# Performance work log

Measured on AMD Instinct MI355X. Metric: run time of the kernel, lower is better.

The kernel has to match this reference:

```python
import jax, jax.numpy as jnp
import numpy as np
import math

NUM_HEADS = 16
ROPE_BASE = 10000.0


def _rope_tables(T, head_dim, dtype=jnp.float32):
    pos = jnp.arange(T, dtype=jnp.float32)
    inv_freq = 1.0 / (ROPE_BASE ** (jnp.arange(0, head_dim, 2, dtype=jnp.float32) / head_dim))
    ang = pos[:, None] * inv_freq[None, :]  # (T, D/2)
    return jnp.cos(ang).astype(dtype), jnp.sin(ang).astype(dtype)


def _apply_rope(x, cos, sin):
    # x: (B, T, H, D); rotate interleaved pairs, position indexed along T
    B, T, H, D = x.shape
    xr = x.reshape(B, T, H, D // 2, 2)
    xe, xo = xr[..., 0], xr[..., 1]
    c = cos[None, :, None, :]  # (1, T, 1, D/2)
    s = sin[None, :, None, :]
    re = xe * c - xo * s
    im = xe * s + xo * c
    return jnp.stack([re, im], axis=-1).reshape(B, T, H, D)


def setup_inputs() -> dict:
    key = jax.random.key(0)
    k1, k2, k3 = jax.random.split(key, 3)
    B, T, C = 2, 2048, 1024
    x = jax.random.normal(k1, (B, T, C), dtype=jnp.float32)
    w_qkv = jax.random.normal(k2, (C, 3 * C), dtype=jnp.float32) * (1.0 / math.sqrt(C))
    w_out = jax.random.normal(k3, (C, C), dtype=jnp.float32) * (1.0 / math.sqrt(C))
    return {"x": x, "w_qkv": w_qkv, "w_out": w_out}


def reference(x, w_qkv, w_out):
    B, T, C = x.shape
    H = NUM_HEADS
    D = C // H
    qkv = jnp.einsum('btc,cf->btf', x, w_qkv)  # (B, T, 3C)
    q, k, v = jnp.split(qkv, 3, axis=-1)
    q = q.reshape(B, T, H, D)
    k = k.reshape(B, T, H, D)
    v = v.reshape(B, T, H, D)
    cos, sin = _rope_tables(T, D)
    q = _apply_rope(q, cos, sin)
    k = _apply_rope(k, cos, sin)
    # (B, H, T, T) scores with causal mask
    att = jnp.einsum('bqhd,bkhd->bhqk', q, k) * (1.0 / math.sqrt(D))
    causal = jnp.tril(jnp.ones((T, T), dtype=bool))
    att = jnp.where(causal[None, None], att, -jnp.inf)
    att = jax.nn.softmax(att, axis=-1)
    out = jnp.einsum('bhqk,bkhd->bqhd', att, v).reshape(B, T, C)
    return jnp.einsum('btc,cd->btd', out, w_out)
```

## Files before the change

kernel.cpp:

```cpp
#include <hip/hip_runtime.h>
#include <stdint.h>


#define B_ 2
#define T_ 2048
#define C_ 1024
#define H_ 16
#define D_ 64
#define F_ 3072
#define M_ 4096

typedef unsigned short u16;
typedef unsigned int u32;
typedef u16 u16x2 __attribute__((ext_vector_type(2)));
typedef u16 u16x4 __attribute__((ext_vector_type(4)));
typedef u16 u16x8 __attribute__((ext_vector_type(8)));
typedef __bf16 bf16x8 __attribute__((ext_vector_type(8)));
typedef float f32x4 __attribute__((ext_vector_type(4)));

__device__ __forceinline__ float b2f(u16 u) {
  union { unsigned int i; float f; } v; v.i = ((unsigned int)u) << 16; return v.f;
}
__device__ __forceinline__ u16 f2b(float f) {
  unsigned int u = __float_as_uint(f);
  u += 0x7fffu + ((u >> 16) & 1u);
  return (u16)(u >> 16);
}
__device__ __forceinline__ bf16x8 u2b8(u16x8 v) {
  union { u16x8 u; bf16x8 b; } x; x.u = v; return x.b;
}


__global__ __launch_bounds__(256) void rope_table_kernel(float* cosT, float* sinT) {
  int idx = blockIdx.x * 256 + threadIdx.x;
  int t = idx >> 5, i = idx & 31;
  float inv_freq = powf(10000.0f, -(float)(2 * i) / 64.0f);
  float ang = (float)t * inv_freq;
  cosT[idx] = cosf(ang);
  sinT[idx] = sinf(ang);
}

__global__ __launch_bounds__(256) void cast_x_kernel(const float* __restrict__ x,
                                                     u16* __restrict__ xb) {
  int i = blockIdx.x * 256 + threadIdx.x;
  float4 v = ((const float4*)x)[i];
  u16x4 r;
  r[0] = f2b(v.x); r[1] = f2b(v.y); r[2] = f2b(v.z); r[3] = f2b(v.w);
  ((u16x4*)xb)[i] = r;
}

__global__ __launch_bounds__(256) void transpose_cast_kernel(const float* __restrict__ in,
                                                             u16* __restrict__ out,
                                                             int R, int Ccol) {
  __shared__ float tile[32][33];
  int c0 = blockIdx.x * 32, r0 = blockIdx.y * 32;
  int tx = threadIdx.x & 31, ty = threadIdx.x >> 5;
  #pragma unroll
  for (int i = 0; i < 32; i += 8)
    tile[ty + i][tx] = in[(size_t)(r0 + ty + i) * Ccol + c0 + tx];
  __syncthreads();
  #pragma unroll
  for (int i = 0; i < 32; i += 8)
    out[(size_t)(c0 + ty + i) * R + r0 + tx] = f2b(tile[tx][ty + i]);
}

template <typename TO>
__global__ __launch_bounds__(256) void gemm_bt_kernel(const u16* __restrict__ A,
                                                      const u16* __restrict__ Bt,
                                                      TO* __restrict__ Cm,
                                                      int M, int N, int K) {
  __shared__ u16 sA[2][128 * 32];
  __shared__ u16 sB[2][128 * 32];
  const int tid = threadIdx.x;
  const int lane = tid & 63;
  const int wv = tid >> 6;
  const int wr = wv >> 1, wc = wv & 1;
  const int l16 = lane & 15, lq = lane >> 4;
  const int rowBase = blockIdx.y * 128;
  const int colBase = blockIdx.x * 128;

  f32x4 acc[4][4] = {};

  const int e0 = wv * 1024 + lane * 8;

#define GSTAGE(buf, kk)                                                          \
  {                                                                              \
    _Pragma("unroll")                                                            \
    for (int s = 0; s < 2; ++s) {                                                \
      int e = e0 + s * 512;                                                      \
      int r = e >> 5, ccc = e & 31;                                              \
      __builtin_amdgcn_global_load_lds(                                          \
          (const __attribute__((address_space(1))) u32*)(A + (size_t)(rowBase + r) * K + (kk) + ccc), \
          (__attribute__((address_space(3))) u32*)&sA[buf][wv * 1024 + s * 512], 16, 0, 0); \
      __builtin_amdgcn_global_load_lds(                                          \
          (const __attribute__((address_space(1))) u32*)(Bt + (size_t)(colBase + r) * K + (kk) + ccc), \
          (__attribute__((address_space(3))) u32*)&sB[buf][wv * 1024 + s * 512], 16, 0, 0); \
    }                                                                            \
  }

  GSTAGE(0, 0);
  asm volatile("s_waitcnt vmcnt(0)" ::: "memory");
  __builtin_amdgcn_s_barrier();

  int cb = 0;
  for (int k0 = 0; k0 < K; k0 += 32, cb ^= 1) {
    const bool more = (k0 + 32 < K);
    if (more) {
      GSTAGE(cb ^ 1, k0 + 32);
      asm volatile("s_waitcnt vmcnt(4)" ::: "memory");
    } else {
      asm volatile("s_waitcnt vmcnt(0)" ::: "memory");
    }
    __builtin_amdgcn_s_barrier();

    bf16x8 af[4], bf[4];
    #pragma unroll
    for (int m = 0; m < 4; ++m)
      af[m] = u2b8(*(const u16x8*)&sA[cb][(wr * 64 + m * 16 + l16) * 32 + lq * 8]);
    #pragma unroll
    for (int n = 0; n < 4; ++n)
      bf[n] = u2b8(*(const u16x8*)&sB[cb][(wc * 64 + n * 16 + l16) * 32 + lq * 8]);
    __builtin_amdgcn_s_setprio(1);
    #pragma unroll
    for (int m = 0; m < 4; ++m)
      #pragma unroll
      for (int n = 0; n < 4; ++n)
        acc[m][n] = __builtin_amdgcn_mfma_f32_16x16x32_bf16(af[m], bf[n], acc[m][n], 0, 0, 0);
    __builtin_amdgcn_s_setprio(0);
    __builtin_amdgcn_s_barrier();
  }
#undef GSTAGE

  #pragma unroll
  for (int m = 0; m < 4; ++m) {
    #pragma unroll
    for (int n = 0; n < 4; ++n) {
      int row = rowBase + wr * 64 + m * 16 + lq * 4;
      int col = colBase + wc * 64 + n * 16 + l16;
      #pragma unroll
      for (int j = 0; j < 4; ++j) {
        float v = acc[m][n][j];
        if constexpr (sizeof(TO) == 2) {
          Cm[(size_t)(row + j) * N + col] = f2b(v);
        } else {
          Cm[(size_t)(row + j) * N + col] = v;
        }
      }
    }
  }
}

__global__ __launch_bounds__(256) void rope_reorg_kernel(const u16* __restrict__ qkv,
                                                         const float* __restrict__ cosT,
                                                         const float* __restrict__ sinT,
                                                         u16* __restrict__ qr,
                                                         u16* __restrict__ kr,
                                                         u16* __restrict__ vr) {
  const float QSC = 0.125f * 1.44269504f;
  int idx = blockIdx.x * 256 + threadIdx.x;
  int d2 = idx & 31;
  int h = (idx >> 5) & 15;
  int t = (idx >> 9) & 2047;
  int b = idx >> 20;
  size_t base = (size_t)(b * T_ + t) * F_ + h * 64 + d2 * 2;
  float qe = b2f(qkv[base]),        qo = b2f(qkv[base + 1]);
  float ke = b2f(qkv[base + C_]),   ko = b2f(qkv[base + C_ + 1]);
  float cv = cosT[t * 32 + d2], sv = sinT[t * 32 + d2];
  size_t ob = ((size_t)(b * H_ + h) * T_ + t) * D_ + d2 * 2;
  qr[ob]     = f2b((qe * cv - qo * sv) * QSC);
  qr[ob + 1] = f2b((qe * sv + qo * cv) * QSC);
  kr[ob]     = f2b(ke * cv - ko * sv);
  kr[ob + 1] = f2b(ke * sv + ko * cv);
  vr[ob]     = qkv[base + 2 * C_];
  vr[ob + 1] = qkv[base + 2 * C_ + 1];
}

__global__ __launch_bounds__(256, 4) void attn_mfma_kernel(const u16* __restrict__ qr,
                                                           const u16* __restrict__ kr,
                                                           const u16* __restrict__ vr,
                                                           u16* __restrict__ ao) {
  constexpr int LDK = 72, LDVT = 72;
  __shared__ u16 sK[2][64 * LDK];
  __shared__ u16 sVt[2][64 * LDVT];

  const int tid = threadIdx.x;
  const int lane = tid & 63;
  const int w = tid >> 6;
  const int l16 = lane & 15, lq = lane >> 4;
  const int bh = blockIdx.x;
  const int qt = (int)gridDim.y - 1 - (int)blockIdx.y;
  const int qbase = qt * 64;
  const size_t hb = (size_t)bh * (T_ * D_);

  bf16x8 qv[2];
  #pragma unroll
  for (int dc = 0; dc < 2; ++dc) {
    int row = qbase + w * 16 + l16;
    qv[dc] = u2b8(*(const u16x8*)(qr + hb + (size_t)row * 64 + dc * 32 + lq * 8));
  }

  f32x4 o[4] = {};
  float mrow = -1e30f;
  float lrow = 0.0f;

  const int skk = tid >> 3;
  const int sd0 = (tid & 7) * 8;
  const int vkp = tid & 31;
  const int vdb = tid >> 5;
  const int vtr = ((vkp >> 4) & 1) * 32 + ((vkp >> 1) & 1) * 16 +
                  ((vkp >> 3) & 1) * 8 + ((vkp >> 2) & 1) * 4 + (vkp & 1) * 2;

  u16x8 rk0, rk1, rv0, rv1;
#define LOADKV(k0)                                                             \
  {                                                                            \
    rk0 = *(const u16x8*)(kr + hb + (size_t)((k0) + skk) * 64 + sd0);          \
    rk1 = *(const u16x8*)(kr + hb + (size_t)((k0) + 32 + skk) * 64 + sd0);     \
    rv0 = *(const u16x8*)(vr + hb + (size_t)((k0) + vtr) * 64 + vdb * 8);      \
    rv1 = *(const u16x8*)(vr + hb + (size_t)((k0) + vtr + 1) * 64 + vdb * 8);  \
  }
#define WRITEKV(buf)                                                           \
  {                                                                            \
    *(u16x8*)&sK[buf][skk * LDK + sd0] = rk0;                                  \
    *(u16x8*)&sK[buf][(32 + skk) * LDK + sd0] = rk1;                           \
    _Pragma("unroll")                                                          \
    for (int u = 0; u < 8; ++u) {                                              \
      u16x2 pk; pk[0] = rv0[u]; pk[1] = rv1[u];                                \
      *(u16x2*)&sVt[buf][(vdb * 8 + u) * LDVT + 2 * vkp] = pk;                 \
    }                                                                          \
  }

  LOADKV(0);
  WRITEKV(0);
  __syncthreads();

  const int nt = qt + 1;
  int cur = 0;
  for (int it = 0; it < nt; ++it) {
    const int k0 = it * 64;
    const bool more = (it + 1 < nt);
    if (more) LOADKV(k0 + 64);

    f32x4 accs[4] = {};
    __builtin_amdgcn_s_setprio(1);
    #pragma unroll
    for (int kt = 0; kt < 4; ++kt) {
      bf16x8 kf0 = u2b8(*(const u16x8*)&sK[cur][(kt * 16 + l16) * LDK + lq * 8]);
      bf16x8 kf1 = u2b8(*(const u16x8*)&sK[cur][(kt * 16 + l16) * LDK + 32 + lq * 8]);
      accs[kt] = __builtin_amdgcn_mfma_f32_16x16x32_bf16(kf0, qv[0], accs[kt], 0, 0, 0);
      accs[kt] = __builtin_amdgcn_mfma_f32_16x16x32_bf16(kf1, qv[1], accs[kt], 0, 0, 0);
    }
    __builtin_amdgcn_s_setprio(0);

    const int qrow = qbase + w * 16 + l16;
    if (k0 + 63 > qbase + w * 16) {
      #pragma unroll
      for (int kt = 0; kt < 4; ++kt)
        #pragma unroll
        for (int j = 0; j < 4; ++j)
          if (k0 + kt * 16 + lq * 4 + j > qrow) accs[kt][j] = -1e30f;
    }
    float m0 = fmaxf(fmaxf(accs[0][0], accs[0][1]), fmaxf(accs[0][2], accs[0][3]));
    float m1 = fmaxf(fmaxf(accs[1][0], accs[1][1]), fmaxf(accs[1][2], accs[1][3]));
    float m2 = fmaxf(fmaxf(accs[2][0], accs[2][1]), fmaxf(accs[2][2], accs[2][3]));
    float m3 = fmaxf(fmaxf(accs[3][0], accs[3][1]), fmaxf(accs[3][2], accs[3][3]));
    float mx = fmaxf(fmaxf(m0, m1), fmaxf(m2, m3));
    mx = fmaxf(mx, __shfl_xor(mx, 16));
    mx = fmaxf(mx, __shfl_xor(mx, 32));

    if (!__all(mx <= mrow)) {
      float mnew = fmaxf(mrow, mx);
      float corr = __builtin_amdgcn_exp2f(mrow - mnew);
      lrow *= corr;
      mrow = mnew;
      f32x4 corrv;
      #pragma unroll
      for (int j = 0; j < 4; ++j) corrv[j] = __shfl(corr, lq * 4 + j);
      #pragma unroll
      for (int dt = 0; dt < 4; ++dt) o[dt] *= corrv;
    }
    const float mu = mrow;
    bf16x8 pb[2];
    float lsum = 0.0f;
    #pragma unroll
    for (int kt = 0; kt < 4; ++kt) {
      #pragma unroll
      for (int j = 0; j < 4; ++j) {
        float p = __builtin_amdgcn_exp2f(accs[kt][j] - mu);
        lsum += p;
        pb[kt >> 1][(kt & 1) * 4 + j] = (__bf16)p;
      }
    }
    lrow += lsum;

    __builtin_amdgcn_s_setprio(1);
    #pragma unroll
    for (int kc = 0; kc < 2; ++kc) {
      #pragma unroll
      for (int dt = 0; dt < 4; ++dt) {
        bf16x8 vt = u2b8(*(const u16x8*)&sVt[cur][(dt * 16 + l16) * LDVT + kc * 32 + lq * 8]);
        o[dt] = __builtin_amdgcn_mfma_f32_16x16x32_bf16(pb[kc], vt, o[dt], 0, 0, 0);
      }
    }
    __builtin_amdgcn_s_setprio(0);

    if (more) WRITEKV(cur ^ 1);
    __syncthreads();
    cur ^= 1;
  }

  const int b = bh >> 4, h = bh & 15;
  float l = lrow;
  l += __shfl_xor(l, 16);
  l += __shfl_xor(l, 32);
  float linv = 1.0f / l;
  #pragma unroll
  for (int j = 0; j < 4; ++j) {
    float lj = __shfl(linv, lq * 4 + j);
    int row = qbase + w * 16 + lq * 4 + j;
    u16* orow = ao + ((size_t)(b * T_ + row)) * C_ + h * 64;
    #pragma unroll
    for (int dt = 0; dt < 4; ++dt)
      orow[dt * 16 + l16] = f2b(o[dt][j] * lj);
  }
}

extern "C" void kernel_launch(void* const* d_in, const int* in_sizes, int n_in,
                              void* d_out, int out_size, void* d_ws, size_t ws_size,
                              hipStream_t stream) {
  const float* x     = (const float*)d_in[0];
  const float* w_qkv = (const float*)d_in[1];
  const float* w_out = (const float*)d_in[2];
  float* out = (float*)d_out;
  char* ws = (char*)d_ws;

  u16* xb     = (u16*)(ws + 0);
  u16* wqkvT  = (u16*)(ws + 8388608);
  u16* woutT  = (u16*)(ws + 14680064);
  u16* qkv    = (u16*)(ws + 16777216);
  u16* qr     = (u16*)(ws + 41943040);
  u16* kr     = (u16*)(ws + 50331648);
  u16* vr     = (u16*)(ws + 58720256);
  u16* ao     = (u16*)(ws + 67108864);
  float* cosT = (float*)(ws + 75497472);
  float* sinT = (float*)(ws + 75759616);

  rope_table_kernel<<<256, 256, 0, stream>>>(cosT, sinT);
  cast_x_kernel<<<4096, 256, 0, stream>>>(x, xb);
  transpose_cast_kernel<<<dim3(96, 32), 256, 0, stream>>>(w_qkv, wqkvT, C_, F_);
  transpose_cast_kernel<<<dim3(32, 32), 256, 0, stream>>>(w_out, woutT, C_, C_);
  gemm_bt_kernel<u16><<<dim3(F_ / 128, M_ / 128), 256, 0, stream>>>(xb, wqkvT, qkv, M_, F_, C_);
  rope_reorg_kernel<<<8192, 256, 0, stream>>>(qkv, cosT, sinT, qr, kr, vr);
  attn_mfma_kernel<<<dim3(B_ * H_, T_ / 64), 256, 0, stream>>>(qr, kr, vr, ao);
  gemm_bt_kernel<float><<<dim3(C_ / 128, M_ / 128), 256, 0, stream>>>(ao, woutT, out, M_, C_, C_);
}
```

Measured before the change: 133.2 us.

## Fuse RoPE and head reorganization into QKV GEMM epilogue; single-buffer attention LDS

The separate rope_reorg kernel is removed. The QKV GEMM epilogue now applies RoPE through lane shuffles and a packed cos/sin table, and writes Q, K and V straight into per-head layout, which drops the bf16 qkv intermediate round trip and one launch. The attention kernel switches from double-buffered to single-buffered K/V shared memory and raises its launch bounds to 8 blocks per SM for occupancy. The price is an extra barrier per iteration and less overlap of loads with compute. The epilogue also writes scattered 2-byte values.

```diff
diff --git a/kernel.cpp b/kernel.cpp
--- a/kernel.cpp
+++ b/kernel.cpp
@@ -31,13 +31,12 @@
 }
 
 
-__global__ __launch_bounds__(256) void rope_table_kernel(float* cosT, float* sinT) {
+__global__ __launch_bounds__(256) void rope_table_kernel(float2* csT) {
   int idx = blockIdx.x * 256 + threadIdx.x;
   int t = idx >> 5, i = idx & 31;
   float inv_freq = powf(10000.0f, -(float)(2 * i) / 64.0f);
   float ang = (float)t * inv_freq;
-  cosT[idx] = cosf(ang);
-  sinT[idx] = sinf(ang);
+  csT[idx] = make_float2(cosf(ang), sinf(ang));
 }
 
 __global__ __launch_bounds__(256) void cast_x_kernel(const float* __restrict__ x,
@@ -64,10 +63,14 @@
     out[(size_t)(c0 + ty + i) * R + r0 + tx] = f2b(tile[tx][ty + i]);
 }
 
-template <typename TO>
+template <int MODE>
 __global__ __launch_bounds__(256) void gemm_bt_kernel(const u16* __restrict__ A,
                                                       const u16* __restrict__ Bt,
-                                                      TO* __restrict__ Cm,
+                                                      float* __restrict__ Cm,
+                                                      u16* __restrict__ qr,
+                                                      u16* __restrict__ kr,
+                                                      u16* __restrict__ vrp,
+                                                      const float2* __restrict__ csT,
                                                       int M, int N, int K) {
   __shared__ u16 sA[2][128 * 32];
   __shared__ u16 sB[2][128 * 32];
@@ -131,57 +134,57 @@
   }
 #undef GSTAGE
 
-  #pragma unroll
-  for (int m = 0; m < 4; ++m) {
-    #pragma unroll
-    for (int n = 0; n < 4; ++n) {
-      int row = rowBase + wr * 64 + m * 16 + lq * 4;
-      int col = colBase + wc * 64 + n * 16 + l16;
-      #pragma unroll
-      for (int j = 0; j < 4; ++j) {
-        float v = acc[m][n][j];
-        if constexpr (sizeof(TO) == 2) {
-          Cm[(size_t)(row + j) * N + col] = f2b(v);
-        } else {
-          Cm[(size_t)(row + j) * N + col] = v;
+  if constexpr (MODE == 0) {
+    #pragma unroll
+    for (int m = 0; m < 4; ++m)
+      #pragma unroll
+      for (int n = 0; n < 4; ++n) {
+        int row = rowBase + wr * 64 + m * 16 + lq * 4;
+        int col = colBase + wc * 64 + n * 16 + l16;
+        #pragma unroll
+        for (int j = 0; j < 4; ++j)
+          Cm[(size_t)(row + j) * N + col] = acc[m][n][j];
+      }
+  } else {
+    const int which = colBase >> 10;
+    const int head = ((colBase + wc * 64) >> 6) & 15;
+    const float QSC = 0.125f * 1.44269504f;
+    u16* const dst = (which == 0) ? qr : (which == 1) ? kr : vrp;
+    #pragma unroll
+    for (int m = 0; m < 4; ++m) {
+      #pragma unroll
+      for (int n = 0; n < 4; ++n) {
+        const int d0 = n * 16 + l16;
+        #pragma unroll
+        for (int j = 0; j < 4; ++j) {
+          int row = rowBase + wr * 64 + m * 16 + lq * 4 + j;
+          int b = row >> 11, t = row & 2047;
+          float v = acc[m][n][j];
+          u16 outv;
+          if (which == 2) {
+            outv = f2b(v);
+          } else {
+            float p = __shfl_xor(v, 1);
+            float2 cs = csT[t * 32 + (d0 >> 1)];
+            float r = (l16 & 1) ? fmaf(p, cs.y, v * cs.x)
+                                : fmaf(-p, cs.y, v * cs.x);
+            if (which == 0) r *= QSC;
+            outv = f2b(r);
+          }
+          dst[((size_t)(b * 16 + head) * 2048 + t) * 64 + d0] = outv;
         }
       }
     }
   }
 }
 
-__global__ __launch_bounds__(256) void rope_reorg_kernel(const u16* __restrict__ qkv,
-                                                         const float* __restrict__ cosT,
-                                                         const float* __restrict__ sinT,
-                                                         u16* __restrict__ qr,
-                                                         u16* __restrict__ kr,
-                                                         u16* __restrict__ vr) {
-  const float QSC = 0.125f * 1.44269504f;
-  int idx = blockIdx.x * 256 + threadIdx.x;
-  int d2 = idx & 31;
-  int h = (idx >> 5) & 15;
-  int t = (idx >> 9) & 2047;
-  int b = idx >> 20;
-  size_t base = (size_t)(b * T_ + t) * F_ + h * 64 + d2 * 2;
-  float qe = b2f(qkv[base]),        qo = b2f(qkv[base + 1]);
-  float ke = b2f(qkv[base + C_]),   ko = b2f(qkv[base + C_ + 1]);
-  float cv = cosT[t * 32 + d2], sv = sinT[t * 32 + d2];
-  size_t ob = ((size_t)(b * H_ + h) * T_ + t) * D_ + d2 * 2;
-  qr[ob]     = f2b((qe * cv - qo * sv) * QSC);
-  qr[ob + 1] = f2b((qe * sv + qo * cv) * QSC);
-  kr[ob]     = f2b(ke * cv - ko * sv);
-  kr[ob + 1] = f2b(ke * sv + ko * cv);
-  vr[ob]     = qkv[base + 2 * C_];
-  vr[ob + 1] = qkv[base + 2 * C_ + 1];
-}
-
-__global__ __launch_bounds__(256, 4) void attn_mfma_kernel(const u16* __restrict__ qr,
+__global__ __launch_bounds__(256, 8) void attn_mfma_kernel(const u16* __restrict__ qr,
                                                            const u16* __restrict__ kr,
                                                            const u16* __restrict__ vr,
                                                            u16* __restrict__ ao) {
   constexpr int LDK = 72, LDVT = 72;
-  __shared__ u16 sK[2][64 * LDK];
-  __shared__ u16 sVt[2][64 * LDVT];
+  __shared__ u16 sK[64 * LDK];
+  __shared__ u16 sVt[64 * LDVT];
 
   const int tid = threadIdx.x;
   const int lane = tid & 63;
@@ -218,23 +221,22 @@
     rv0 = *(const u16x8*)(vr + hb + (size_t)((k0) + vtr) * 64 + vdb * 8);      \
     rv1 = *(const u16x8*)(vr + hb + (size_t)((k0) + vtr + 1) * 64 + vdb * 8);  \
   }
-#define WRITEKV(buf)                                                           \
+#define WRITEKV()                                                              \
   {                                                                            \
-    *(u16x8*)&sK[buf][skk * LDK + sd0] = rk0;                                  \
-    *(u16x8*)&sK[buf][(32 + skk) * LDK + sd0] = rk1;                           \
+    *(u16x8*)&sK[skk * LDK + sd0] = rk0;                                       \
+    *(u16x8*)&sK[(32 + skk) * LDK + sd0] = rk1;                                \
     _Pragma("unroll")                                                          \
     for (int u = 0; u < 8; ++u) {                                              \
       u16x2 pk; pk[0] = rv0[u]; pk[1] = rv1[u];                                \
-      *(u16x2*)&sVt[buf][(vdb * 8 + u) * LDVT + 2 * vkp] = pk;                 \
+      *(u16x2*)&sVt[(vdb * 8 + u) * LDVT + 2 * vkp] = pk;                      \
     }                                                                          \
   }
 
   LOADKV(0);
-  WRITEKV(0);
+  WRITEKV();
   __syncthreads();
 
   const int nt = qt + 1;
-  int cur = 0;
   for (int it = 0; it < nt; ++it) {
     const int k0 = it * 64;
     const bool more = (it + 1 < nt);
@@ -244,8 +246,8 @@
     __builtin_amdgcn_s_setprio(1);
     #pragma unroll
     for (int kt = 0; kt < 4; ++kt) {
-      bf16x8 kf0 = u2b8(*(const u16x8*)&sK[cur][(kt * 16 + l16) * LDK + lq * 8]);
-      bf16x8 kf1 = u2b8(*(const u16x8*)&sK[cur][(kt * 16 + l16) * LDK + 32 + lq * 8]);
+      bf16x8 kf0 = u2b8(*(const u16x8*)&sK[(kt * 16 + l16) * LDK + lq * 8]);
+      bf16x8 kf1 = u2b8(*(const u16x8*)&sK[(kt * 16 + l16) * LDK + 32 + lq * 8]);
       accs[kt] = __builtin_amdgcn_mfma_f32_16x16x32_bf16(kf0, qv[0], accs[kt], 0, 0, 0);
       accs[kt] = __builtin_amdgcn_mfma_f32_16x16x32_bf16(kf1, qv[1], accs[kt], 0, 0, 0);
     }
@@ -297,15 +299,17 @@
     for (int kc = 0; kc < 2; ++kc) {
       #pragma unroll
       for (int dt = 0; dt < 4; ++dt) {
-        bf16x8 vt = u2b8(*(const u16x8*)&sVt[cur][(dt * 16 + l16) * LDVT + kc * 32 + lq * 8]);
+        bf16x8 vt = u2b8(*(const u16x8*)&sVt[(dt * 16 + l16) * LDVT + kc * 32 + lq * 8]);
         o[dt] = __builtin_amdgcn_mfma_f32_16x16x32_bf16(pb[kc], vt, o[dt], 0, 0, 0);
       }
     }
     __builtin_amdgcn_s_setprio(0);
 
-    if (more) WRITEKV(cur ^ 1);
     __syncthreads();
-    cur ^= 1;
+    if (more) {
+      WRITEKV();
+      __syncthreads();
+    }
   }
 
   const int b = bh >> 4, h = bh & 15;
@@ -336,20 +340,19 @@
   u16* xb     = (u16*)(ws + 0);
   u16* wqkvT  = (u16*)(ws + 8388608);
   u16* woutT  = (u16*)(ws + 14680064);
-  u16* qkv    = (u16*)(ws + 16777216);
   u16* qr     = (u16*)(ws + 41943040);
   u16* kr     = (u16*)(ws + 50331648);
   u16* vr     = (u16*)(ws + 58720256);
   u16* ao     = (u16*)(ws + 67108864);
-  float* cosT = (float*)(ws + 75497472);
-  float* sinT = (float*)(ws + 75759616);
-
-  rope_table_kernel<<<256, 256, 0, stream>>>(cosT, sinT);
+  float2* csT = (float2*)(ws + 75497472);
+
+  rope_table_kernel<<<256, 256, 0, stream>>>(csT);
   cast_x_kernel<<<4096, 256, 0, stream>>>(x, xb);
   transpose_cast_kernel<<<dim3(96, 32), 256, 0, stream>>>(w_qkv, wqkvT, C_, F_);
   transpose_cast_kernel<<<dim3(32, 32), 256, 0, stream>>>(w_out, woutT, C_, C_);
-  gemm_bt_kernel<u16><<<dim3(F_ / 128, M_ / 128), 256, 0, stream>>>(xb, wqkvT, qkv, M_, F_, C_);
-  rope_reorg_kernel<<<8192, 256, 0, stream>>>(qkv, cosT, sinT, qr, kr, vr);
+  gemm_bt_kernel<2><<<dim3(F_ / 128, M_ / 128), 256, 0, stream>>>(
+      xb, wqkvT, nullptr, qr, kr, vr, (const float2*)csT, M_, F_, C_);
   attn_mfma_kernel<<<dim3(B_ * H_, T_ / 64), 256, 0, stream>>>(qr, kr, vr, ao);
-  gemm_bt_kernel<float><<<dim3(C_ / 128, M_ / 128), 256, 0, stream>>>(ao, woutT, out, M_, C_, C_);
-}
+  gemm_bt_kernel<0><<<dim3(C_ / 128, M_ / 128), 256, 0, stream>>>(
+      ao, woutT, out, nullptr, nullptr, nullptr, nullptr, M_, C_, C_);
+}
```

Measured after the change: 232.2 us. +74.3%, slower.
